# Kernel optimization log

Hardware: AMD Instinct MI355X
Metric: run time of the kernel (lower is better)

## Reference

```python
import jax, jax.numpy as jnp
import numpy as np

K_NN = 16

def knn_idx(x, k):
    # x: (B, N, 3); FoldingNet-style: topk of negative squared distance (self included)
    xx = jnp.sum(x * x, axis=-1)                      # (B, N)
    inner = jnp.einsum('bnd,bmd->bnm', x, x)          # (B, N, N)
    neg_dist = -(xx[:, :, None] - 2.0 * inner + xx[:, None, :])
    _, idx = jax.lax.top_k(neg_dist, k)               # (B, N, k)
    return idx

def local_cov(x, idx):
    # x: (B, N, 3), idx: (B, N, k); uses neighbors 0 and 1 only (as in FoldingNet local_cov)
    B = x.shape[0]
    b = jnp.arange(B)[:, None, None]
    nbr = x[b, idx[:, :, :2]]                         # (B, N, 2, 3)
    outer = nbr[:, :, 0, :, None] * nbr[:, :, 1, None, :]   # (B, N, 3, 3)
    outer = outer.reshape(B, x.shape[1], 9)
    return jnp.concatenate([x, outer], axis=-1)       # (B, N, 12)

def mlp(x, wa, ba, wr, br, wo, bo):
    # Linear -> ReLU -> Residual_Linear_Layer -> ReLU -> Linear
    h = jax.nn.relu(x @ wa + ba)
    h = jax.nn.relu(h + (h @ wr + br))
    return h @ wo + bo

def setup_inputs() -> dict:
    key = jax.random.key(0)
    B, N, F = 16, 2048, 512
    ks = jax.random.split(key, 24)
    inp = {
        'latent': jax.random.normal(ks[0], (B, N, F), jnp.float32),
        'recon_pc': jax.random.normal(ks[1], (B, N, 3), jnp.float32),
    }
    def lin(k, din, dout):
        s = 1.0 / np.sqrt(din)
        k1, k2 = jax.random.split(k)
        return (jax.random.uniform(k1, (din, dout), jnp.float32, -s, s),
                jax.random.uniform(k2, (dout,), jnp.float32, -s, s))
    i = 2
    for s, din0 in [(1, F + 12), (2, F + 1), (3, F + 1)]:
        inp[f'w{s}a'], inp[f'b{s}a'] = lin(ks[i], din0, F); i += 1
        inp[f'w{s}r'], inp[f'b{s}r'] = lin(ks[i], F, F); i += 1
        inp[f'w{s}o'], inp[f'b{s}o'] = lin(ks[i], F, 1); i += 1
    return inp

def reference(latent, recon_pc,
              w1a, b1a, w1r, b1r, w1o, b1o,
              w2a, b2a, w2r, b2r, w2o, b2o,
              w3a, b3a, w3r, b3r, w3o, b3o):
    idx = knn_idx(recon_pc, K_NN)                     # (B, N, k)
    cov = local_cov(recon_pc, idx)                    # (B, N, 12)
    out = mlp(jnp.concatenate([latent, cov], axis=-1), w1a, b1a, w1r, b1r, w1o, b1o)
    out = out + mlp(jnp.concatenate([latent, out], axis=-1), w2a, b2a, w2r, b2r, w2o, b2o)
    out = out + mlp(jnp.concatenate([latent, out], axis=-1), w3a, b3a, w3r, b3r, w3o, b3o)
    return out                                        # (B, N, 1)
```

## Files before the change

### kernel.cpp

```cpp
#include <hip/hip_runtime.h>
#include <hip/hip_bf16.h>

typedef __attribute__((ext_vector_type(8))) short short8;
typedef __attribute__((ext_vector_type(4))) float f32x4;

__device__ __forceinline__ short bf16r(float f) {
    union { float f; unsigned u; } v; v.f = f;
    unsigned u = (v.u + 0x7fffu + ((v.u >> 16) & 1u)) >> 16;
    return (short)u;
}
__device__ __forceinline__ float bf2f(short s) {
    union { unsigned u; float f; } v; v.u = ((unsigned)(unsigned short)s) << 16;
    return v.f;
}

__device__ __forceinline__ int fswz(int r) { return (r ^ (r >> 2)) & 3; }

__device__ __forceinline__ void gl16(const short* g, short* l) {
    __builtin_amdgcn_global_load_lds(
        (const __attribute__((address_space(1))) unsigned int*)g,
        (__attribute__((address_space(3))) unsigned int*)l, 16, 0, 0);
}

#define M_ROWS 32768
#define KP_A 544
#define NF 512

__global__ __launch_bounds__(256) void k_latent(const float* __restrict__ latent,
                                                short* __restrict__ A) {
    int idx = blockIdx.x * 256 + threadIdx.x;
    int row = idx >> 6;
    int c = (idx & 63) << 3;
    const float* src = latent + (long)row * NF + c;
    float4 f0 = *(const float4*)src;
    float4 f1 = *(const float4*)(src + 4);
    short8 o;
    o[0] = bf16r(f0.x); o[1] = bf16r(f0.y); o[2] = bf16r(f0.z); o[3] = bf16r(f0.w);
    o[4] = bf16r(f1.x); o[5] = bf16r(f1.y); o[6] = bf16r(f1.z); o[7] = bf16r(f1.w);
    *(short8*)(A + (long)row * KP_A + c) = o;
}

__global__ __launch_bounds__(256) void k_wt6(const float* __restrict__ w0,
                                             const float* __restrict__ w1,
                                             const float* __restrict__ w2,
                                             const float* __restrict__ w3,
                                             const float* __restrict__ w4,
                                             const float* __restrict__ w5,
                                             short* __restrict__ wdst) {
    int z = blockIdx.z;
    const float* W = (z == 0) ? w0 : (z == 1) ? w1 : (z == 2) ? w2
                   : (z == 3) ? w3 : (z == 4) ? w4 : w5;
    int din = (z == 0) ? 524 : 512;
    int Kp  = (z < 3) ? KP_A : NF;
    short* Wt = wdst + ((z < 3) ? (size_t)z * NF * KP_A
                                : (size_t)3 * NF * KP_A + (size_t)(z - 3) * NF * NF);
    int kt = blockIdx.x * 32;
    if (kt >= Kp) return;
    int nt = blockIdx.y * 32;
    __shared__ float tile[32][33];
    int tx = threadIdx.x & 31, ty = threadIdx.x >> 5;
    #pragma unroll
    for (int r = 0; r < 32; r += 8) {
        int k = kt + ty + r;
        tile[ty + r][tx] = (k < din) ? W[(long)k * NF + nt + tx] : 0.0f;
    }
    __syncthreads();
    #pragma unroll
    for (int r = 0; r < 32; r += 8) {
        int n = nt + ty + r, k = kt + tx;
        Wt[(long)n * Kp + k] = bf16r(tile[tx][ty + r]);
    }
}

__device__ __forceinline__ bool beats(float va, int ia, float vb, int ib) {
    return va > vb || (va == vb && ia < ib);
}

__global__ __launch_bounds__(256, 2) void k_knncov(const float* __restrict__ pc,
                                                   short* __restrict__ A) {
    __shared__ float sx[2048], sy[2048], sz[2048], sq[2048];
    __shared__ int ires[32];
    int b = blockIdx.x >> 7;
    int chunk = blockIdx.x & 127;
    const float* p = pc + (long)b * 2048 * 3;
    for (int i = threadIdx.x; i < 2048; i += 256) {
        float x = p[3 * i], y = p[3 * i + 1], z = p[3 * i + 2];
        sx[i] = x; sy[i] = y; sz[i] = z;
        sq[i] = x * x + y * y + z * z;
    }
    __syncthreads();
    int wid = threadIdx.x >> 6, lane = threadIdx.x & 63;
    int nbase = chunk * 16 + wid * 4;

    float qx[4], qy[4], qz[4], qq[4];
    #pragma unroll
    for (int i = 0; i < 4; ++i) {
        qx[i] = sx[nbase + i]; qy[i] = sy[nbase + i];
        qz[i] = sz[nbase + i]; qq[i] = sq[nbase + i];
    }
    float b0[4], b1[4]; int j0[4], j1[4];
    #pragma unroll
    for (int i = 0; i < 4; ++i) { b0[i] = -INFINITY; b1[i] = -INFINITY; j0[i] = 0; j1[i] = 0; }

    for (int it = 0; it < 32; ++it) {
        int m = it * 64 + lane;
        float mx = sx[m], my = sy[m], mz = sz[m], mq = sq[m];
        #pragma unroll
        for (int i = 0; i < 4; ++i) {
            float inner = qx[i] * mx + qy[i] * my + qz[i] * mz;
            float negd = -((qq[i] - 2.0f * inner) + mq);
            bool c0 = negd > b0[i];
            bool c1 = negd > b1[i];
            float t1 = c0 ? b0[i] : (c1 ? negd : b1[i]);
            int   u1 = c0 ? j0[i] : (c1 ? m : j1[i]);
            b1[i] = t1; j1[i] = u1;
            b0[i] = c0 ? negd : b0[i];
            j0[i] = c0 ? m : j0[i];
        }
    }

    #pragma unroll
    for (int i = 0; i < 4; ++i) {
        float v0 = b0[i], v1 = b1[i]; int k0 = j0[i], k1 = j1[i];
        #pragma unroll
        for (int off = 1; off < 64; off <<= 1) {
            float w0 = __shfl_xor(v0, off, 64), w1 = __shfl_xor(v1, off, 64);
            int   l0 = __shfl_xor(k0, off, 64), l1 = __shfl_xor(k1, off, 64);
            float n0v, n1v; int n0i, n1i;
            if (beats(v0, k0, w0, l0)) {
                n0v = v0; n0i = k0;
                if (beats(w0, l0, v1, k1)) { n1v = w0; n1i = l0; } else { n1v = v1; n1i = k1; }
            } else {
                n0v = w0; n0i = l0;
                if (beats(v0, k0, w1, l1)) { n1v = v0; n1i = k0; } else { n1v = w1; n1i = l1; }
            }
            v0 = n0v; k0 = n0i; v1 = n1v; k1 = n1i;
        }
        if (lane == 0) {
            ires[wid * 8 + i * 2]     = k0;
            ires[wid * 8 + i * 2 + 1] = k1;
        }
    }
    __syncthreads();
    if (threadIdx.x < 16) {
        int t = threadIdx.x;
        int k0 = ires[(t >> 2) * 8 + (t & 3) * 2];
        int k1 = ires[(t >> 2) * 8 + (t & 3) * 2 + 1];
        int n = chunk * 16 + t;
        float xn = sx[n], yn = sy[n], zn = sz[n];
        float a0 = sx[k0], a1 = sy[k0], a2 = sz[k0];
        float c0 = sx[k1], c1 = sy[k1], c2 = sz[k1];
        long row = (long)b * 2048 + n;
        short vals[32];
        vals[0] = bf16r(xn); vals[1] = bf16r(yn); vals[2] = bf16r(zn);
        float ou[9] = {a0 * c0, a0 * c1, a0 * c2,
                       a1 * c0, a1 * c1, a1 * c2,
                       a2 * c0, a2 * c1, a2 * c2};
        #pragma unroll
        for (int q = 0; q < 9; ++q) vals[3 + q] = bf16r(ou[q]);
        #pragma unroll
        for (int q = 12; q < 32; ++q) vals[q] = 0;
        short* dst = A + row * KP_A + NF;
        #pragma unroll
        for (int q = 0; q < 4; ++q)
            *(short8*)(dst + q * 8) = *(short8*)(vals + q * 8);
    }
}

__global__ __launch_bounds__(256) void k_setbo(float* __restrict__ out,
                                               const float* __restrict__ bo, int add) {
    int i = blockIdx.x * 256 + threadIdx.x;
    float v = bo[0];
    out[i] = add ? (out[i] + v) : v;
}

#define BM 256
#define BN 128
#define BK 32

__global__ __launch_bounds__(512, 4) void k_gemm(const short* __restrict__ A,
                                                 const short* __restrict__ Bt,
                                                 const float* __restrict__ bias,
                                                 const short* __restrict__ Res,
                                                 short* __restrict__ C,
                                                 const float* __restrict__ wov,
                                                 float* __restrict__ outp,
                                                 const float* __restrict__ wex,
                                                 const float* __restrict__ outv,
                                                 const float* __restrict__ bov,
                                                 int lda, int kend) {
    __shared__ __align__(16) short As[3][BM * BK];
    __shared__ __align__(16) short Bs[3][BN * BK];
    int nwg = gridDim.x;
    int orig = blockIdx.x;
    int wgid = (orig & 7) * (nwg >> 3) + (orig >> 3);
    int bm = wgid >> 2, bn = wgid & 3;
    int t = threadIdx.x, lane = t & 63, wid = t >> 6;
    int wm = wid >> 1, wn = wid & 1;
    f32x4 acc[4][4] = {};
    const long arow0 = (long)bm * BM, brow0 = (long)bn * BN;
    int l15 = lane & 15;

    int rcA0 = (wid * 2) * 16 + (lane >> 2);
    int rcA1 = (wid * 2 + 1) * 16 + (lane >> 2);
    int rcB  = wid * 16 + (lane >> 2);
    int ksA0 = ((lane & 3) ^ fswz(rcA0)) * 8;
    int ksA1 = ((lane & 3) ^ fswz(rcA1)) * 8;
    int ksB  = ((lane & 3) ^ fswz(rcB)) * 8;
    long aoff0 = (arow0 + rcA0) * (long)lda + ksA0;
    long aoff1 = (arow0 + rcA1) * (long)lda + ksA1;
    long boff  = (brow0 + rcB) * (long)lda + ksB;
    int cbA0 = (wid * 2) * 512;
    int cbA1 = (wid * 2 + 1) * 512;
    int cbB  = wid * 512;

    int ra[4], rb[4];
    #pragma unroll
    for (int i = 0; i < 4; ++i) {
        int rA = wm * 64 + i * 16 + l15;
        int rB = wn * 64 + i * 16 + l15;
        ra[i] = rA * 32 + (((lane >> 4) ^ fswz(rA)) * 8);
        rb[i] = rB * 32 + (((lane >> 4) ^ fswz(rB)) * 8);
    }

#define STAGE(bufi, ktoff) do { \
        gl16(A  + aoff0 + (ktoff), &As[bufi][cbA0]); \
        gl16(A  + aoff1 + (ktoff), &As[bufi][cbA1]); \
        gl16(Bt + boff  + (ktoff), &Bs[bufi][cbB]); \
    } while (0)

    int nt = kend / BK;
    STAGE(0, 0);
    STAGE(1, BK);
    asm volatile("s_waitcnt vmcnt(3)" ::: "memory");
    __builtin_amdgcn_sched_barrier(0);
    __builtin_amdgcn_s_barrier();

    int cur = 0;
    for (int kt = 0; kt < nt; ++kt) {
        short8 fa[4], fb[4];
        #pragma unroll
        for (int i = 0; i < 4; ++i) {
            fa[i] = *(const short8*)&As[cur][ra[i]];
            fb[i] = *(const short8*)&Bs[cur][rb[i]];
        }
        if (kt + 2 < nt) {
            int stg = (cur >= 1) ? cur - 1 : 2;
            STAGE(stg, (kt + 2) * BK);
            asm volatile("s_waitcnt vmcnt(3) lgkmcnt(0)" ::: "memory");
            __builtin_amdgcn_sched_barrier(0);
            __builtin_amdgcn_s_barrier();
        } else if (kt + 1 < nt) {
            asm volatile("s_waitcnt vmcnt(0) lgkmcnt(0)" ::: "memory");
            __builtin_amdgcn_sched_barrier(0);
            __builtin_amdgcn_s_barrier();
        }
        __builtin_amdgcn_s_setprio(1);
        #pragma unroll
        for (int i = 0; i < 4; ++i)
            #pragma unroll
            for (int j = 0; j < 4; ++j)
                acc[i][j] = __builtin_amdgcn_mfma_f32_16x16x32_bf16(fa[i], fb[j], acc[i][j], 0, 0, 0);
        __builtin_amdgcn_s_setprio(0);
        cur = (cur >= 2) ? 0 : cur + 1;
    }
#undef STAGE

    int rq4 = (lane >> 4) * 4;
    if (wov == nullptr) {
        #pragma unroll
        for (int i = 0; i < 4; ++i) {
            #pragma unroll
            for (int j = 0; j < 4; ++j) {
                int col = bn * BN + wn * 64 + j * 16 + l15;
                float bval = bias[col];
                float wexv = wex ? wex[col] : 0.0f;
                #pragma unroll
                for (int r = 0; r < 4; ++r) {
                    long row = arow0 + wm * 64 + i * 16 + rq4 + r;
                    float v = acc[i][j][r] + bval;
                    if (wex) v += outv[row] * wexv;
                    v = fmaxf(v, 0.0f);
                    C[row * NF + col] = bf16r(v);
                }
            }
        }
    } else {
        float wv[4], bv[4];
        #pragma unroll
        for (int j = 0; j < 4; ++j) {
            int col = bn * BN + wn * 64 + j * 16 + l15;
            wv[j] = wov[col];
            bv[j] = bias[col];
        }
        float boadd = (bov != nullptr && wn == 0 && bn == 0) ? bov[0] : 0.0f;
        #pragma unroll
        for (int i = 0; i < 4; ++i) {
            #pragma unroll
            for (int r = 0; r < 4; ++r) {
                long row = arow0 + wm * 64 + i * 16 + rq4 + r;
                float s = 0.0f;
                #pragma unroll
                for (int j = 0; j < 4; ++j) {
                    int col = bn * BN + wn * 64 + j * 16 + l15;
                    float v = acc[i][j][r] + bv[j] + bf2f(Res[row * NF + col]);
                    v = fmaxf(v, 0.0f);
                    s += v * wv[j];
                }
                s += __shfl_xor(s, 1, 64);
                s += __shfl_xor(s, 2, 64);
                s += __shfl_xor(s, 4, 64);
                s += __shfl_xor(s, 8, 64);
                if (l15 == 0) atomicAdd(outp + row, s + boadd);
            }
        }
    }
}

extern "C" void kernel_launch(void* const* d_in, const int* in_sizes, int n_in,
                              void* d_out, int out_size, void* d_ws, size_t ws_size,
                              hipStream_t stream) {
    (void)in_sizes; (void)n_in; (void)out_size; (void)ws_size;
    const float* latent = (const float*)d_in[0];
    const float* pc     = (const float*)d_in[1];
    const float *wa[3], *ba[3], *wr[3], *br[3], *wo[3], *bo[3];
    for (int s = 0; s < 3; ++s) {
        int base = 2 + s * 6;
        wa[s] = (const float*)d_in[base + 0];
        ba[s] = (const float*)d_in[base + 1];
        wr[s] = (const float*)d_in[base + 2];
        br[s] = (const float*)d_in[base + 3];
        wo[s] = (const float*)d_in[base + 4];
        bo[s] = (const float*)d_in[base + 5];
    }

    char* ws = (char*)d_ws;
    size_t off = 0;
    short* A  = (short*)(ws + off); off += (size_t)M_ROWS * KP_A * 2;
    short* H1 = (short*)(ws + off); off += (size_t)M_ROWS * NF * 2;
    short* Wbase = (short*)(ws + off);
    short *Wta[3], *Wtr[3];
    for (int s = 0; s < 3; ++s) { Wta[s] = Wbase + (size_t)s * NF * KP_A; }
    for (int s = 0; s < 3; ++s) { Wtr[s] = Wbase + (size_t)3 * NF * KP_A + (size_t)s * NF * NF; }
    float* out = (float*)d_out;

    k_latent<<<(M_ROWS * 64) / 256, 256, 0, stream>>>(latent, A);
    dim3 gw((KP_A + 31) / 32, NF / 32, 6);
    k_wt6<<<gw, 256, 0, stream>>>(wa[0], wa[1], wa[2], wr[0], wr[1], wr[2], Wbase);
    k_knncov<<<2048, 256, 0, stream>>>(pc, A);
    k_setbo<<<M_ROWS / 256, 256, 0, stream>>>(out, bo[0], 0);

    int nwg = (M_ROWS / BM) * (NF / BN);
    for (int s = 0; s < 3; ++s) {
        if (s == 0) {
            k_gemm<<<nwg, 512, 0, stream>>>(A, Wta[0], ba[0], nullptr, H1,
                                            nullptr, nullptr, nullptr, nullptr,
                                            nullptr, KP_A, KP_A);
        } else {
            k_gemm<<<nwg, 512, 0, stream>>>(A, Wta[s], ba[s], nullptr, H1,
                                            nullptr, nullptr,
                                            wa[s] + (size_t)NF * NF, out,
                                            nullptr, KP_A, NF);
        }
        k_gemm<<<nwg, 512, 0, stream>>>(H1, Wtr[s], br[s], H1, nullptr,
                                        wo[s], out, nullptr, nullptr,
                                        s > 0 ? bo[s] : nullptr, NF, NF);
    }
}
```

Before: 224.5 us.

## Interleave LDS fragment reads with MFMAs and slim the kNN top-2 kernel

The GEMM main loop now issues the next-stage global-to-LDS prefetch first, then loads A fragments one row at a time between MFMA groups. The wait and barrier move to the end of the iteration, so LDS reads overlap matrix math and the barrier no longer sits between the fragment loads and the MFMAs. Separately, the kNN kernel drops the shared squared-norm array and recomputes norms in registers. It uses fmax/fmin for the top-2 value update and asks for 4 blocks per CU instead of 2. The occupancy request may force more register pressure, and the new MFMA ordering depends on the compiler scheduling the interleaved LDS reads well.

```diff
diff --git a/kernel.cpp b/kernel.cpp
--- a/kernel.cpp
+++ b/kernel.cpp
@@ -76,17 +76,15 @@
     return va > vb || (va == vb && ia < ib);
 }
 
-__global__ __launch_bounds__(256, 2) void k_knncov(const float* __restrict__ pc,
+__global__ __launch_bounds__(256, 4) void k_knncov(const float* __restrict__ pc,
                                                    short* __restrict__ A) {
-    __shared__ float sx[2048], sy[2048], sz[2048], sq[2048];
+    __shared__ float sx[2048], sy[2048], sz[2048];
     __shared__ int ires[32];
     int b = blockIdx.x >> 7;
     int chunk = blockIdx.x & 127;
     const float* p = pc + (long)b * 2048 * 3;
     for (int i = threadIdx.x; i < 2048; i += 256) {
-        float x = p[3 * i], y = p[3 * i + 1], z = p[3 * i + 2];
-        sx[i] = x; sy[i] = y; sz[i] = z;
-        sq[i] = x * x + y * y + z * z;
+        sx[i] = p[3 * i]; sy[i] = p[3 * i + 1]; sz[i] = p[3 * i + 2];
     }
     __syncthreads();
     int wid = threadIdx.x >> 6, lane = threadIdx.x & 63;
@@ -95,8 +93,8 @@
     float qx[4], qy[4], qz[4], qq[4];
     #pragma unroll
     for (int i = 0; i < 4; ++i) {
-        qx[i] = sx[nbase + i]; qy[i] = sy[nbase + i];
-        qz[i] = sz[nbase + i]; qq[i] = sq[nbase + i];
+        qx[i] = sx[nbase + i]; qy[i] = sy[nbase + i]; qz[i] = sz[nbase + i];
+        qq[i] = qx[i] * qx[i] + qy[i] * qy[i] + qz[i] * qz[i];
     }
     float b0[4], b1[4]; int j0[4], j1[4];
     #pragma unroll
@@ -104,18 +102,18 @@
 
     for (int it = 0; it < 32; ++it) {
         int m = it * 64 + lane;
-        float mx = sx[m], my = sy[m], mz = sz[m], mq = sq[m];
+        float mx = sx[m], my = sy[m], mz = sz[m];
+        float mq = mx * mx + my * my + mz * mz;
         #pragma unroll
         for (int i = 0; i < 4; ++i) {
             float inner = qx[i] * mx + qy[i] * my + qz[i] * mz;
             float negd = -((qq[i] - 2.0f * inner) + mq);
             bool c0 = negd > b0[i];
             bool c1 = negd > b1[i];
-            float t1 = c0 ? b0[i] : (c1 ? negd : b1[i]);
-            int   u1 = c0 ? j0[i] : (c1 ? m : j1[i]);
-            b1[i] = t1; j1[i] = u1;
-            b0[i] = c0 ? negd : b0[i];
+            j1[i] = c0 ? j0[i] : (c1 ? m : j1[i]);
+            b1[i] = fmaxf(b1[i], fminf(b0[i], negd));
             j0[i] = c0 ? m : j0[i];
+            b0[i] = fmaxf(b0[i], negd);
         }
     }
 
@@ -238,30 +236,31 @@
 
     int cur = 0;
     for (int kt = 0; kt < nt; ++kt) {
-        short8 fa[4], fb[4];
-        #pragma unroll
-        for (int i = 0; i < 4; ++i) {
-            fa[i] = *(const short8*)&As[cur][ra[i]];
-            fb[i] = *(const short8*)&Bs[cur][rb[i]];
-        }
         if (kt + 2 < nt) {
             int stg = (cur >= 1) ? cur - 1 : 2;
             STAGE(stg, (kt + 2) * BK);
-            asm volatile("s_waitcnt vmcnt(3) lgkmcnt(0)" ::: "memory");
+        }
+        short8 fb[4];
+        #pragma unroll
+        for (int j = 0; j < 4; ++j) fb[j] = *(const short8*)&Bs[cur][rb[j]];
+        __builtin_amdgcn_s_setprio(1);
+        #pragma unroll
+        for (int i = 0; i < 4; ++i) {
+            short8 fa = *(const short8*)&As[cur][ra[i]];
+            #pragma unroll
+            for (int j = 0; j < 4; ++j)
+                acc[i][j] = __builtin_amdgcn_mfma_f32_16x16x32_bf16(fa, fb[j], acc[i][j], 0, 0, 0);
+        }
+        __builtin_amdgcn_s_setprio(0);
+        if (kt + 1 < nt) {
+            if (kt + 2 < nt) {
+                asm volatile("s_waitcnt vmcnt(3) lgkmcnt(0)" ::: "memory");
+            } else {
+                asm volatile("s_waitcnt vmcnt(0) lgkmcnt(0)" ::: "memory");
+            }
             __builtin_amdgcn_sched_barrier(0);
             __builtin_amdgcn_s_barrier();
-        } else if (kt + 1 < nt) {
-            asm volatile("s_waitcnt vmcnt(0) lgkmcnt(0)" ::: "memory");
-            __builtin_amdgcn_sched_barrier(0);
-            __builtin_amdgcn_s_barrier();
-        }
-        __builtin_amdgcn_s_setprio(1);
-        #pragma unroll
-        for (int i = 0; i < 4; ++i)
-            #pragma unroll
-            for (int j = 0; j < 4; ++j)
-                acc[i][j] = __builtin_amdgcn_mfma_f32_16x16x32_bf16(fa[i], fb[j], acc[i][j], 0, 0, 0);
-        __builtin_amdgcn_s_setprio(0);
+        }
         cur = (cur >= 2) ? 0 : cur + 1;
     }
 #undef STAGE
```

Measured after the change: 234.2 us. +4.3%, slower.
